# Optimization experiments

Measured on AMD Instinct MI355X. Metric: run time of the kernel, lower is better.

The kernel has to match this reference:

```python
import jax, jax.numpy as jnp
import numpy as np

EPS = 1e-12
NUM_HEADS = 16
FEATURE_DIM = 16
HEAD_DIM = 64


def setup_inputs() -> dict:
    key = jax.random.key(0)
    k1, k2, k3, k4, k5 = jax.random.split(key, 5)
    b, l, d_model = 2, 2048, 1024
    scale = 0.02
    return {
        "hidden_states": jax.random.normal(k1, (b, l, d_model), jnp.float32),
        "Wq": jax.random.normal(k2, (FEATURE_DIM * NUM_HEADS, d_model), jnp.float32) * scale,
        "Wk": jax.random.normal(k3, (FEATURE_DIM * NUM_HEADS, d_model), jnp.float32) * scale,
        "Wv": jax.random.normal(k4, (NUM_HEADS * HEAD_DIM, d_model), jnp.float32) * scale,
        "Wo": jax.random.normal(k5, (d_model, NUM_HEADS * HEAD_DIM), jnp.float32) * scale,
    }


def reference(hidden_states, Wq, Wk, Wv, Wo):
    b, l, d_model = hidden_states.shape
    h, fd, hd = NUM_HEADS, FEATURE_DIM, HEAD_DIM
    # projections (no bias), split heads: (b, h, l, dim)
    q = (hidden_states @ Wq.T).reshape(b, l, h, fd).transpose(0, 2, 1, 3)
    k = (hidden_states @ Wk.T).reshape(b, l, h, fd).transpose(0, 2, 1, 3)
    v = (hidden_states @ Wv.T).reshape(b, l, h, hd).transpose(0, 2, 1, 3)
    # feature map is identity (default FeatureMap)
    # quadratic causal linear attention
    A_qk = jnp.einsum("bhnd,bhmd->bhnm", q, k)  # [b,h,l,l]
    A_qk = jnp.tril(A_qk)
    y = jnp.einsum("bhnm,bhme->bhne", A_qk, v)  # [b,h,l,hd]
    # denominator: q . cumsum(k)
    z = 1.0 / (jnp.einsum("bhld,bhld->bhl", q, jnp.cumsum(k, axis=2)) + EPS)
    y = y * z[..., None]
    # merge heads and output projection
    y = y.transpose(0, 2, 1, 3).reshape(b, l, h * hd)
    return y @ Wo.T
```

## Files before the change

### kernel.cpp

```cpp
#include <hip/hip_runtime.h>
#include <hip/hip_bf16.h>

#define NH 16
#define FD 16
#define HD 64
#define BATCH 2
#define SEQ 2048
#define DM 1024
#define ROWS (BATCH * SEQ)
#define CHUNK 128
#define NCH (SEQ / CHUNK)
#define NBH (BATCH * NH)

typedef __hip_bfloat16 bf16;
typedef __attribute__((ext_vector_type(8))) short short8;
typedef __attribute__((ext_vector_type(4))) float f32x4;

__device__ inline float bfbits(unsigned int h) {
  union { unsigned int u; float f; } c; c.u = h << 16; return c.f;
}
__device__ inline unsigned short f2bf(float x) {
  bf16 h = __float2bfloat16(x);
  return *(unsigned short*)&h;
}

__device__ inline void load8(const void* src, size_t idx, int isf32, float* out) {
  if (isf32) {
    const float* p = (const float*)src + idx;
    float4 a = *(const float4*)p;
    float4 b = *(const float4*)(p + 4);
    out[0] = a.x; out[1] = a.y; out[2] = a.z; out[3] = a.w;
    out[4] = b.x; out[5] = b.y; out[6] = b.z; out[7] = b.w;
  } else {
    const uint4 w = *(const uint4*)((const unsigned short*)src + idx);
    out[0] = bfbits(w.x & 0xffffu); out[1] = bfbits(w.x >> 16);
    out[2] = bfbits(w.y & 0xffffu); out[3] = bfbits(w.y >> 16);
    out[4] = bfbits(w.z & 0xffffu); out[5] = bfbits(w.z >> 16);
    out[6] = bfbits(w.w & 0xffffu); out[7] = bfbits(w.w >> 16);
  }
}

__device__ inline void gload16(const void* g, void* l) {
  __builtin_amdgcn_global_load_lds(
      (const __attribute__((address_space(1))) unsigned int*)g,
      (__attribute__((address_space(3))) unsigned int*)l, 16, 0, 0);
}

__global__ __launch_bounds__(256) void detect_dtype(const unsigned int* __restrict__ w,
                                                    int* __restrict__ flag) {
  __shared__ int red[256];
  int cnt = 0;
  for (int i = threadIdx.x; i < 4096; i += 256) {
    unsigned int e = (w[i] >> 7) & 0xFFu;
    cnt += (e >= 0x90u) ? 1 : 0;
  }
  red[threadIdx.x] = cnt;
  __syncthreads();
  for (int s = 128; s > 0; s >>= 1) {
    if (threadIdx.x < s) red[threadIdx.x] += red[threadIdx.x + s];
    __syncthreads();
  }
  if (threadIdx.x == 0) *flag = (red[0] > 64) ? 1 : 0;
}

__global__ __launch_bounds__(256) void gemm_qk3(const void* __restrict__ A,
                                                const void* __restrict__ Wq,
                                                const void* __restrict__ Wk,
                                                const int* __restrict__ flagp,
                                                float* __restrict__ qf,
                                                float* __restrict__ kf) {
  const int isf32 = *flagp;
  __shared__ float As[64][36];
  __shared__ float Bs[64][36];
  const int tid = threadIdx.x;
  const int m0 = blockIdx.x * 64;
  const int isK = blockIdx.y >> 2;
  const int n0 = (blockIdx.y & 3) * 64;
  const void* B = isK ? Wk : Wq;
  float* C = isK ? kf : qf;
  const int tx = tid & 15, ty = tid >> 4;
  const int lm = tid >> 2, lc = (tid & 3) * 8;
  double dacc[4][4];
#pragma unroll
  for (int i = 0; i < 4; ++i)
#pragma unroll
    for (int j = 0; j < 4; ++j) dacc[i][j] = 0.0;

  for (int kt = 0; kt < DM; kt += 32) {
    float av[8], bv[8];
    load8(A, (size_t)(m0 + lm) * DM + kt + lc, isf32, av);
    load8(B, (size_t)(n0 + lm) * DM + kt + lc, isf32, bv);
    __syncthreads();
    *(float4*)&As[lm][lc] = *(float4*)&av[0];
    *(float4*)&As[lm][lc + 4] = *(float4*)&av[4];
    *(float4*)&Bs[lm][lc] = *(float4*)&bv[0];
    *(float4*)&Bs[lm][lc + 4] = *(float4*)&bv[4];
    __syncthreads();
    for (int kk = 0; kk < 32; kk += 4) {
      float4 ar[4], br[4];
#pragma unroll
      for (int i = 0; i < 4; ++i) ar[i] = *(const float4*)&As[tx + 16 * i][kk];
#pragma unroll
      for (int n = 0; n < 4; ++n) br[n] = *(const float4*)&Bs[ty * 4 + n][kk];
      float facc[4][4] = {};
#pragma unroll
      for (int j = 0; j < 4; ++j) {
#pragma unroll
        for (int i = 0; i < 4; ++i) {
          float a = ((const float*)&ar[i])[j];
#pragma unroll
          for (int n = 0; n < 4; ++n)
            facc[i][n] += a * ((const float*)&br[n])[j];
        }
      }
#pragma unroll
      for (int i = 0; i < 4; ++i)
#pragma unroll
        for (int n = 0; n < 4; ++n) dacc[i][n] += (double)facc[i][n];
    }
  }
#pragma unroll
  for (int i = 0; i < 4; ++i) {
    int row = m0 + tx + 16 * i;
    float4 o;
    o.x = (float)dacc[i][0]; o.y = (float)dacc[i][1];
    o.z = (float)dacc[i][2]; o.w = (float)dacc[i][3];
    *(float4*)&C[(size_t)row * 256 + n0 + ty * 4] = o;
  }
}

template <int MODE>
__global__ __launch_bounds__(256) void gemm_mfma(const void* __restrict__ Ap,
                                                 const void* __restrict__ Bp,
                                                 const int* __restrict__ flagp,
                                                 void* __restrict__ Cp) {
  const int isf32 = *flagp;
  const int aF32 = (MODE == 0) ? isf32 : 0;
  const int bF32 = isf32;
  __shared__ unsigned short As[128 * 32];
  __shared__ unsigned short Bs[64 * 32];
  const int tid = threadIdx.x;
  const int wave = tid >> 6, lane = tid & 63;
  const int m0 = blockIdx.x * 128, n0 = blockIdx.y * 64;
  const int lrow = lane >> 2, lch = (lane & 3) * 8;
  const int wm = wave >> 1, wn = wave & 1;
  const int mlane = lane & 15, kgrp = lane >> 4;
  const unsigned short* Ab = (const unsigned short*)Ap;
  const unsigned short* Bb = (const unsigned short*)Bp;
  f32x4 acc[4][2];
#pragma unroll
  for (int t = 0; t < 4; ++t)
#pragma unroll
    for (int u = 0; u < 2; ++u) acc[t][u] = (f32x4){0.f, 0.f, 0.f, 0.f};

  for (int k0 = 0; k0 < DM; k0 += 32) {
    __syncthreads();
    if (!aF32) {
      const int r0 = wave * 32;
#pragma unroll
      for (int j = 0; j < 2; ++j) {
        const void* g = Ab + (size_t)(m0 + r0 + j * 16 + lrow) * DM + k0 + lch;
        gload16(g, &As[(r0 + j * 16) * 32]);
      }
    } else {
      for (int c = tid; c < 512; c += 256) {
        int r = c >> 2, cc = (c & 3) * 8;
        float v8[8];
        load8(Ap, (size_t)(m0 + r) * DM + k0 + cc, 1, v8);
        unsigned int w[4];
#pragma unroll
        for (int g2 = 0; g2 < 4; ++g2)
          w[g2] = (unsigned)f2bf(v8[2 * g2]) | ((unsigned)f2bf(v8[2 * g2 + 1]) << 16);
        *(uint4*)&As[r * 32 + cc] = *(uint4*)w;
      }
    }
    if (!bF32) {
      const void* g = Bb + (size_t)(n0 + wave * 16 + lrow) * DM + k0 + lch;
      gload16(g, &Bs[(wave * 16) * 32]);
    } else {
      {
        int c = tid;
        int r = c >> 2, cc = (c & 3) * 8;
        float v8[8];
        load8(Bp, (size_t)(n0 + r) * DM + k0 + cc, 1, v8);
        unsigned int w[4];
#pragma unroll
        for (int g2 = 0; g2 < 4; ++g2)
          w[g2] = (unsigned)f2bf(v8[2 * g2]) | ((unsigned)f2bf(v8[2 * g2 + 1]) << 16);
        *(uint4*)&Bs[r * 32 + cc] = *(uint4*)w;
      }
    }
    __syncthreads();

    short8 af[4], bfr[2];
#pragma unroll
    for (int t = 0; t < 4; ++t)
      af[t] = *(const short8*)&As[(wm * 64 + t * 16 + mlane) * 32 + kgrp * 8];
#pragma unroll
    for (int u = 0; u < 2; ++u)
      bfr[u] = *(const short8*)&Bs[(wn * 32 + u * 16 + mlane) * 32 + kgrp * 8];
#pragma unroll
    for (int t = 0; t < 4; ++t)
#pragma unroll
      for (int u = 0; u < 2; ++u)
        acc[t][u] = __builtin_amdgcn_mfma_f32_16x16x32_bf16(af[t], bfr[u], acc[t][u], 0, 0, 0);
  }

#pragma unroll
  for (int t = 0; t < 4; ++t)
#pragma unroll
    for (int u = 0; u < 2; ++u)
#pragma unroll
      for (int r = 0; r < 4; ++r) {
        int row = m0 + wm * 64 + t * 16 + kgrp * 4 + r;
        int col = n0 + wn * 32 + u * 16 + mlane;
        float v = acc[t][u][r];
        if (MODE == 0) {
          ((unsigned short*)Cp)[(size_t)row * DM + col] = f2bf(v);
        } else if (isf32) {
          ((float*)Cp)[(size_t)row * DM + col] = v;
        } else {
          ((unsigned short*)Cp)[(size_t)row * DM + col] = f2bf(v);
        }
      }
}

__global__ __launch_bounds__(256) void attn_intra(const float* __restrict__ qf,
                                                  const float* __restrict__ kf,
                                                  const unsigned short* __restrict__ vfb,
                                                  unsigned short* __restrict__ yib,
                                                  float* __restrict__ Sc,
                                                  double* __restrict__ Kc) {
  __shared__ float qc[CHUNK][20];
  __shared__ float kc[CHUNK][20];
  __shared__ float vc[CHUNK][68];
  const int bh = blockIdx.x >> 4;
  const int c = blockIdx.x & 15;
  const int b = bh >> 4, h = bh & 15;
  const int bl = c * CHUNK;
  const int tid = threadIdx.x;

  for (int idx = tid; idx < CHUNK * FD / 4; idx += 256) {
    int r = idx >> 2, f4 = (idx & 3) * 4;
    size_t g = ((size_t)(b * SEQ + bl + r)) * (NH * FD) + h * FD + f4;
    *(float4*)&qc[r][f4] = *(const float4*)&qf[g];
    *(float4*)&kc[r][f4] = *(const float4*)&kf[g];
  }
  for (int idx = tid; idx < CHUNK * HD / 8; idx += 256) {
    int r = idx >> 3, e8 = (idx & 7) * 8;
    uint4 w = *(const uint4*)&vfb[((size_t)(b * SEQ + bl + r)) * (NH * HD) + h * HD + e8];
    vc[r][e8 + 0] = bfbits(w.x & 0xffffu); vc[r][e8 + 1] = bfbits(w.x >> 16);
    vc[r][e8 + 2] = bfbits(w.y & 0xffffu); vc[r][e8 + 3] = bfbits(w.y >> 16);
    vc[r][e8 + 4] = bfbits(w.z & 0xffffu); vc[r][e8 + 5] = bfbits(w.z >> 16);
    vc[r][e8 + 6] = bfbits(w.w & 0xffffu); vc[r][e8 + 7] = bfbits(w.w >> 16);
  }
  __syncthreads();

  const int p = tid >> 2;
  const int n0 = 2 * p, n1 = 2 * p + 1;
  const int e0 = (tid & 3) * 16;
  float q0r[16], q1r[16];
#pragma unroll
  for (int d = 0; d < 16; ++d) { q0r[d] = qc[n0][d]; q1r[d] = qc[n1][d]; }
  float y0[16], y1[16];
#pragma unroll
  for (int e = 0; e < 16; ++e) { y0[e] = 0.f; y1[e] = 0.f; }

  for (int m = 0; m <= n1; ++m) {
    float kd[16], vv[16];
#pragma unroll
    for (int d = 0; d < 16; ++d) kd[d] = kc[m][d];
#pragma unroll
    for (int e = 0; e < 16; ++e) vv[e] = vc[m][e0 + e];
    float d0 = 0.f, d1 = 0.f;
#pragma unroll
    for (int d = 0; d < 16; ++d) { d0 += q0r[d] * kd[d]; d1 += q1r[d] * kd[d]; }
    if (m > n0) d0 = 0.f;
#pragma unroll
    for (int e = 0; e < 16; ++e) { y0[e] += d0 * vv[e]; y1[e] += d1 * vv[e]; }
  }
  const size_t ybase = (size_t)bh * SEQ + bl;
  {
    unsigned int w[4];
#pragma unroll
    for (int g = 0; g < 4; ++g)
      w[g] = (unsigned)f2bf(y0[2 * g]) | ((unsigned)f2bf(y0[2 * g + 1]) << 16);
    *(uint4*)&yib[(ybase + n0) * HD + e0] = *(uint4*)w;
#pragma unroll
    for (int g = 0; g < 4; ++g)
      w[g] = (unsigned)f2bf(y0[8 + 2 * g]) | ((unsigned)f2bf(y0[9 + 2 * g]) << 16);
    *(uint4*)&yib[(ybase + n0) * HD + e0 + 8] = *(uint4*)w;
#pragma unroll
    for (int g = 0; g < 4; ++g)
      w[g] = (unsigned)f2bf(y1[2 * g]) | ((unsigned)f2bf(y1[2 * g + 1]) << 16);
    *(uint4*)&yib[(ybase + n1) * HD + e0] = *(uint4*)w;
#pragma unroll
    for (int g = 0; g < 4; ++g)
      w[g] = (unsigned)f2bf(y1[8 + 2 * g]) | ((unsigned)f2bf(y1[9 + 2 * g]) << 16);
    *(uint4*)&yib[(ybase + n1) * HD + e0 + 8] = *(uint4*)w;
  }

  float* Scp = Sc + ((size_t)bh * NCH + c) * (FD * HD);
  for (int idx = tid; idx < FD * HD; idx += 256) {
    int d = idx >> 6, e = idx & 63;
    float s = 0.f;
    for (int m = 0; m < CHUNK; ++m) s += kc[m][d] * vc[m][e];
    Scp[idx] = s;
  }
  if (tid < FD) {
    double ks = 0.0;
    for (int m = 0; m < CHUNK; ++m) ks += (double)kc[m][tid];
    Kc[((size_t)bh * NCH + c) * FD + tid] = ks;
  }
}

__global__ __launch_bounds__(256) void scan_states(float* __restrict__ Sc,
                                                   double* __restrict__ Kc) {
  const int bh = blockIdx.x;
  const int tid = threadIdx.x;
  float4 acc = make_float4(0.f, 0.f, 0.f, 0.f);
  size_t base = (size_t)bh * NCH * (FD * HD) + (size_t)tid * 4;
  for (int c = 0; c < NCH; ++c) {
    float4* p = (float4*)(Sc + base + (size_t)c * (FD * HD));
    float4 v = *p;
    *p = acc;
    acc.x += v.x; acc.y += v.y; acc.z += v.z; acc.w += v.w;
  }
  if (tid < FD) {
    double a = 0.0;
    for (int c = 0; c < NCH; ++c) {
      size_t i = ((size_t)bh * NCH + c) * FD + tid;
      double t = Kc[i];
      Kc[i] = a;
      a += t;
    }
  }
}

__global__ __launch_bounds__(256) void attn_finish(const float* __restrict__ qf,
                                                   const float* __restrict__ kf,
                                                   const unsigned short* __restrict__ yib,
                                                   const float* __restrict__ Sc,
                                                   const double* __restrict__ Kc,
                                                   unsigned short* __restrict__ yob) {
  __shared__ float qc[CHUNK][20];
  __shared__ float kc[CHUNK][20];
  __shared__ float Sp[FD][HD];
  __shared__ double cs[CHUNK][17];
  __shared__ double zl[CHUNK];
  __shared__ double ksp[FD];
  const int bh = blockIdx.x >> 4;
  const int c = blockIdx.x & 15;
  const int b = bh >> 4, h = bh & 15;
  const int bl = c * CHUNK;
  const int tid = threadIdx.x;

  for (int idx = tid; idx < CHUNK * FD / 4; idx += 256) {
    int r = idx >> 2, f4 = (idx & 3) * 4;
    size_t g = ((size_t)(b * SEQ + bl + r)) * (NH * FD) + h * FD + f4;
    *(float4*)&qc[r][f4] = *(const float4*)&qf[g];
    *(float4*)&kc[r][f4] = *(const float4*)&kf[g];
  }
  const float* Scp = Sc + ((size_t)bh * NCH + c) * (FD * HD);
  for (int idx = tid; idx < FD * HD / 4; idx += 256) {
    int d = idx >> 4, e4 = (idx & 15) * 4;
    *(float4*)&Sp[d][e4] = *(const float4*)&Scp[(size_t)d * HD + e4];
  }
  if (tid < FD) ksp[tid] = Kc[((size_t)bh * NCH + c) * FD + tid];
  __syncthreads();

  if (tid < FD) {
    double run = ksp[tid];
    for (int m = 0; m < CHUNK; ++m) {
      run += (double)kc[m][tid];
      cs[m][tid] = run;
    }
  }
  __syncthreads();
  if (tid < CHUNK) {
    double dn = 0.0;
#pragma unroll
    for (int d = 0; d < 16; ++d) dn += (double)qc[tid][d] * cs[tid][d];
    zl[tid] = 1.0 / (dn + 1e-12);
  }
  __syncthreads();

  for (int idx = tid; idx < CHUNK * HD / 8; idx += 256) {
    int n = idx >> 3, e8 = (idx & 7) * 8;
    uint4 w = *(const uint4*)&yib[((size_t)bh * SEQ + bl + n) * HD + e8];
    float yv[8] = {bfbits(w.x & 0xffffu), bfbits(w.x >> 16),
                   bfbits(w.y & 0xffffu), bfbits(w.y >> 16),
                   bfbits(w.z & 0xffffu), bfbits(w.z >> 16),
                   bfbits(w.w & 0xffffu), bfbits(w.w >> 16)};
    double z = zl[n];
    unsigned int o[4];
#pragma unroll
    for (int jp = 0; jp < 4; ++jp) {
      int e = e8 + 2 * jp;
      float i0 = 0.f, i1 = 0.f;
#pragma unroll
      for (int d = 0; d < 16; ++d) {
        i0 += qc[n][d] * Sp[d][e];
        i1 += qc[n][d] * Sp[d][e + 1];
      }
      float r0 = (float)(((double)(yv[2 * jp] + i0)) * z);
      float r1 = (float)(((double)(yv[2 * jp + 1] + i1)) * z);
      o[jp] = (unsigned)f2bf(r0) | ((unsigned)f2bf(r1) << 16);
    }
    *(uint4*)&yob[((size_t)(b * SEQ + bl + n)) * (NH * HD) + h * HD + e8] = *(uint4*)o;
  }
}

extern "C" void kernel_launch(void* const* d_in, const int* in_sizes, int n_in,
                              void* d_out, int out_size, void* d_ws, size_t ws_size,
                              hipStream_t stream) {
  (void)in_sizes; (void)n_in; (void)out_size; (void)ws_size;
  const void* hs = d_in[0];
  const void* Wq = d_in[1];
  const void* Wk = d_in[2];
  const void* Wv = d_in[3];
  const void* Wo = d_in[4];

  char* ws = (char*)d_ws;
  float* qf = (float*)(ws);
  float* kf = (float*)(ws + (4u << 20));
  unsigned short* vfb = (unsigned short*)(ws + (8u << 20));
  unsigned short* yob = vfb;
  unsigned short* yib = (unsigned short*)(ws + (16u << 20));
  float* Sc = (float*)(ws + (24u << 20));
  double* Kc = (double*)(ws + (26u << 20));
  int* flag = (int*)(ws + (26u << 20) + 65536);

  detect_dtype<<<1, 256, 0, stream>>>((const unsigned int*)hs, flag);
  gemm_qk3<<<dim3(ROWS / 64, 8), 256, 0, stream>>>(hs, Wq, Wk, flag, qf, kf);
  gemm_mfma<0><<<dim3(ROWS / 128, 1024 / 64), 256, 0, stream>>>(hs, Wv, flag, vfb);
  attn_intra<<<NBH * NCH, 256, 0, stream>>>(qf, kf, vfb, yib, Sc, Kc);
  scan_states<<<NBH, 256, 0, stream>>>(Sc, Kc);
  attn_finish<<<NBH * NCH, 256, 0, stream>>>(qf, kf, yib, Sc, Kc, yob);
  gemm_mfma<1><<<dim3(ROWS / 128, 1024 / 64), 256, 0, stream>>>(yob, Wo, flag, d_out);
}
```

Before: 307.3 us.

## Enlarge Q/K projection tile to 128 rows and prefetch next K-slice into registers

```diff
diff --git a/kernel.cpp b/kernel.cpp
--- a/kernel.cpp
+++ b/kernel.cpp
@@ -63,50 +63,60 @@
   if (threadIdx.x == 0) *flag = (red[0] > 64) ? 1 : 0;
 }
 
-__global__ __launch_bounds__(256) void gemm_qk3(const void* __restrict__ A,
+__global__ __launch_bounds__(256) void gemm_qk4(const void* __restrict__ A,
                                                 const void* __restrict__ Wq,
                                                 const void* __restrict__ Wk,
                                                 const int* __restrict__ flagp,
                                                 float* __restrict__ qf,
                                                 float* __restrict__ kf) {
   const int isf32 = *flagp;
-  __shared__ float As[64][36];
-  __shared__ float Bs[64][36];
+  __shared__ float As[128 * 36];
+  __shared__ float Bs[64 * 36];
   const int tid = threadIdx.x;
-  const int m0 = blockIdx.x * 64;
+  const int m0 = blockIdx.x * 128;
   const int isK = blockIdx.y >> 2;
   const int n0 = (blockIdx.y & 3) * 64;
   const void* B = isK ? Wk : Wq;
   float* C = isK ? kf : qf;
   const int tx = tid & 15, ty = tid >> 4;
-  const int lm = tid >> 2, lc = (tid & 3) * 8;
-  double dacc[4][4];
-#pragma unroll
-  for (int i = 0; i < 4; ++i)
-#pragma unroll
-    for (int j = 0; j < 4; ++j) dacc[i][j] = 0.0;
+  const int lmA = tid >> 1, lcA = (tid & 1) * 16;
+  const int lmB = tid >> 2, lcB = (tid & 3) * 8;
+  double dacc[8][4];
+#pragma unroll
+  for (int i = 0; i < 8; ++i)
+#pragma unroll
+    for (int n = 0; n < 4; ++n) dacc[i][n] = 0.0;
+
+  float av[16], bv[8];
+  load8(A, (size_t)(m0 + lmA) * DM + lcA, isf32, &av[0]);
+  load8(A, (size_t)(m0 + lmA) * DM + lcA + 8, isf32, &av[8]);
+  load8(B, (size_t)(n0 + lmB) * DM + lcB, isf32, bv);
 
   for (int kt = 0; kt < DM; kt += 32) {
-    float av[8], bv[8];
-    load8(A, (size_t)(m0 + lm) * DM + kt + lc, isf32, av);
-    load8(B, (size_t)(n0 + lm) * DM + kt + lc, isf32, bv);
     __syncthreads();
-    *(float4*)&As[lm][lc] = *(float4*)&av[0];
-    *(float4*)&As[lm][lc + 4] = *(float4*)&av[4];
-    *(float4*)&Bs[lm][lc] = *(float4*)&bv[0];
-    *(float4*)&Bs[lm][lc + 4] = *(float4*)&bv[4];
+    *(float4*)&As[lmA * 36 + lcA] = *(float4*)&av[0];
+    *(float4*)&As[lmA * 36 + lcA + 4] = *(float4*)&av[4];
+    *(float4*)&As[lmA * 36 + lcA + 8] = *(float4*)&av[8];
+    *(float4*)&As[lmA * 36 + lcA + 12] = *(float4*)&av[12];
+    *(float4*)&Bs[lmB * 36 + lcB] = *(float4*)&bv[0];
+    *(float4*)&Bs[lmB * 36 + lcB + 4] = *(float4*)&bv[4];
     __syncthreads();
+    if (kt + 32 < DM) {
+      load8(A, (size_t)(m0 + lmA) * DM + kt + 32 + lcA, isf32, &av[0]);
+      load8(A, (size_t)(m0 + lmA) * DM + kt + 32 + lcA + 8, isf32, &av[8]);
+      load8(B, (size_t)(n0 + lmB) * DM + kt + 32 + lcB, isf32, bv);
+    }
     for (int kk = 0; kk < 32; kk += 4) {
-      float4 ar[4], br[4];
-#pragma unroll
-      for (int i = 0; i < 4; ++i) ar[i] = *(const float4*)&As[tx + 16 * i][kk];
-#pragma unroll
-      for (int n = 0; n < 4; ++n) br[n] = *(const float4*)&Bs[ty * 4 + n][kk];
-      float facc[4][4] = {};
+      float4 ar[8], br[4];
+#pragma unroll
+      for (int i = 0; i < 8; ++i) ar[i] = *(const float4*)&As[(tx + 16 * i) * 36 + kk];
+#pragma unroll
+      for (int n = 0; n < 4; ++n) br[n] = *(const float4*)&Bs[(ty * 4 + n) * 36 + kk];
+      float facc[8][4] = {};
 #pragma unroll
       for (int j = 0; j < 4; ++j) {
 #pragma unroll
-        for (int i = 0; i < 4; ++i) {
+        for (int i = 0; i < 8; ++i) {
           float a = ((const float*)&ar[i])[j];
 #pragma unroll
           for (int n = 0; n < 4; ++n)
@@ -114,13 +124,13 @@
         }
       }
 #pragma unroll
-      for (int i = 0; i < 4; ++i)
+      for (int i = 0; i < 8; ++i)
 #pragma unroll
         for (int n = 0; n < 4; ++n) dacc[i][n] += (double)facc[i][n];
     }
   }
 #pragma unroll
-  for (int i = 0; i < 4; ++i) {
+  for (int i = 0; i < 8; ++i) {
     int row = m0 + tx + 16 * i;
     float4 o;
     o.x = (float)dacc[i][0]; o.y = (float)dacc[i][1];
@@ -432,7 +442,7 @@
   int* flag = (int*)(ws + (26u << 20) + 65536);
 
   detect_dtype<<<1, 256, 0, stream>>>((const unsigned int*)hs, flag);
-  gemm_qk3<<<dim3(ROWS / 64, 8), 256, 0, stream>>>(hs, Wq, Wk, flag, qf, kf);
+  gemm_qk4<<<dim3(ROWS / 128, 8), 256, 0, stream>>>(hs, Wq, Wk, flag, qf, kf);
   gemm_mfma<0><<<dim3(ROWS / 128, 1024 / 64), 256, 0, stream>>>(hs, Wv, flag, vfb);
   attn_intra<<<NBH * NCH, 256, 0, stream>>>(qf, kf, vfb, yib, Sc, Kc);
   scan_states<<<NBH, 256, 0, stream>>>(Sc, Kc);
```

Measured after the change: 319.9 us. 1.04x slower.
